# Performance work log

Measured on AMD Instinct MI355X. Metric: run time of the kernel, lower is better.

The kernel has to match this reference:

```python
import jax, jax.numpy as jnp
import numpy as np

N_HIDDEN = 512
N_MOTIF_PER_CLASS = 16
N_CLASS = 10
N_MOTIF = N_MOTIF_PER_CLASS * N_CLASS
TEMPERATURE = 0.2
EPS = 1e-4


def setup_inputs() -> dict:
    key = jax.random.key(0)
    k1, k2, k3 = jax.random.split(key, 3)
    B = 65536
    z = jax.random.normal(k1, (B, N_HIDDEN), dtype=jnp.float32)
    M = jax.random.normal(k2, (N_MOTIF, N_HIDDEN), dtype=jnp.float32)
    y = jax.random.randint(k3, (B,), 0, N_CLASS, dtype=jnp.int64)
    return {"z": z, "M": M, "y": y}


def reference(z, M, y):
    # euclidean_1 similarity: squared euclidean distance + log-ratio transform
    xp = z @ M.T                                     # [B, n_motif]
    dist = -2.0 * xp + jnp.sum(z * z, axis=1, keepdims=True) \
           + jnp.sum(M * M, axis=1)[None, :]         # [B, n_motif]
    similarity = jnp.log((dist + 1.0) / (dist + EPS))

    sims = jnp.exp(similarity / TEMPERATURE)          # [B, n_motif]

    # true_motifs mask: motif j belongs to class j // n_motif_per_class
    motif_class = jnp.arange(N_MOTIF) // N_MOTIF_PER_CLASS   # [n_motif]
    pos_mask = (motif_class[None, :] == y[:, None])           # [B, n_motif] bool

    # positives are contiguous per row, so the torch boolean-index reshape
    # is equivalent to a masked row-sum
    sim_pos = jnp.sum(jnp.where(pos_mask, sims, 0.0), axis=1)  # [B]
    sim_neg = jnp.sum(jnp.where(pos_mask, 0.0, sims), axis=1)  # [B]

    loss = -jnp.mean(jnp.log(sim_pos / (sim_neg + sim_pos)))
    return loss
```

## Files before the change

### kernel.cpp

```cpp
#include <hip/hip_runtime.h>
#include <math.h>

#define NH 512
#define NM 160
#define BROWS 65536
#define BM 128
#define BK 64
#define NCHUNK (NH / BK)

typedef __attribute__((ext_vector_type(8))) __bf16 bf16x8;
typedef __attribute__((ext_vector_type(4))) __bf16 bf16x4;
typedef __attribute__((ext_vector_type(4))) float  f32x4;

__global__ __launch_bounds__(64) void mprep_kernel(const float* __restrict__ M,
                                                   __bf16* __restrict__ Mb,
                                                   float* __restrict__ mnorm) {
    const int m = blockIdx.x;
    const int l = threadIdx.x;
    const float* row = M + (size_t)m * NH;
    float s = 0.f;
#pragma unroll
    for (int k = 0; k < 2; ++k) {
        float4 v = *reinterpret_cast<const float4*>(row + 4 * l + 256 * k);
        s = fmaf(v.x, v.x, fmaf(v.y, v.y, fmaf(v.z, v.z, fmaf(v.w, v.w, s))));
        bf16x4 b = {(__bf16)v.x, (__bf16)v.y, (__bf16)v.z, (__bf16)v.w};
        *reinterpret_cast<bf16x4*>(Mb + (size_t)m * NH + 4 * l + 256 * k) = b;
    }
#pragma unroll
    for (int off = 32; off > 0; off >>= 1) s += __shfl_down(s, off);
    if (l == 0) mnorm[m] = s;
}

__global__ __launch_bounds__(256, 2) void motif_main(
    const float* __restrict__ z, const __bf16* __restrict__ Mb,
    const int* __restrict__ y, const float* __restrict__ mnorm,
    float* __restrict__ loss_sum) {
    __shared__ __align__(16) __bf16 zs[BM * BK];
    __shared__ __align__(16) __bf16 ms[NM * BK];
    __shared__ float znorm[BM];
    __shared__ float red[256];

    const int tid = threadIdx.x;
    const int w   = tid >> 6;
    const int l   = tid & 63;
    const int row0 = blockIdx.x * BM;

    f32x4 acc[2][10];
#pragma unroll
    for (int rt = 0; rt < 2; ++rt)
#pragma unroll
        for (int ct = 0; ct < 10; ++ct) acc[rt][ct] = (f32x4){0.f, 0.f, 0.f, 0.f};
    float zp[8] = {0.f, 0.f, 0.f, 0.f, 0.f, 0.f, 0.f, 0.f};

#pragma unroll 1
    for (int ch = 0; ch < NCHUNK; ++ch) {
        const int k0 = ch * BK;
#pragma unroll
        for (int s = 0; s < 8; ++s) {
            const int idx = tid + 256 * s;
            const int r = idx >> 4, c4 = idx & 15;
            float4 v = *reinterpret_cast<const float4*>(
                z + (size_t)(row0 + r) * NH + k0 + c4 * 4);
            zp[s] = fmaf(v.x, v.x, fmaf(v.y, v.y, fmaf(v.z, v.z, fmaf(v.w, v.w, zp[s]))));
            const int slot = (c4 >> 1) ^ (r & 7);
            bf16x4 b = {(__bf16)v.x, (__bf16)v.y, (__bf16)v.z, (__bf16)v.w};
            *reinterpret_cast<bf16x4*>(&zs[r * BK + slot * 8 + (c4 & 1) * 4]) = b;
        }
#pragma unroll
        for (int s = 0; s < 5; ++s) {
            const int sidx = tid + 256 * s;
            const int r = sidx >> 3, sl = sidx & 7;
            bf16x8 v = *reinterpret_cast<const bf16x8*>(
                Mb + (size_t)r * NH + k0 + sl * 8);
            *reinterpret_cast<bf16x8*>(&ms[r * BK + (sl ^ (r & 7)) * 8]) = v;
        }
        __syncthreads();

        const int r16 = l & 15;
        const int kg  = l >> 4;
#pragma unroll
        for (int q = 0; q < 2; ++q) {
            const int slotk = q * 4 + kg;
            bf16x8 a[2], b[10];
#pragma unroll
            for (int rt = 0; rt < 2; ++rt) {
                const int r = w * 32 + rt * 16 + r16;
                a[rt] = *reinterpret_cast<const bf16x8*>(
                    &zs[r * BK + (slotk ^ (r & 7)) * 8]);
            }
#pragma unroll
            for (int ct = 0; ct < 10; ++ct) {
                const int r = ct * 16 + r16;
                b[ct] = *reinterpret_cast<const bf16x8*>(
                    &ms[r * BK + (slotk ^ (r & 7)) * 8]);
            }
#pragma unroll
            for (int rt = 0; rt < 2; ++rt)
#pragma unroll
                for (int ct = 0; ct < 10; ++ct)
                    acc[rt][ct] = __builtin_amdgcn_mfma_f32_16x16x32_bf16(
                        a[rt], b[ct], acc[rt][ct], 0, 0, 0);
        }
        __syncthreads();
    }

#pragma unroll
    for (int s = 0; s < 8; ++s) {
#pragma unroll
        for (int off = 1; off < 16; off <<= 1) zp[s] += __shfl_xor(zp[s], off);
    }
    if ((l & 15) == 0) {
#pragma unroll
        for (int s = 0; s < 8; ++s) znorm[(tid >> 4) + 16 * s] = zp[s];
    }
    __syncthreads();

    float mn[10];
#pragma unroll
    for (int ct = 0; ct < 10; ++ct) mn[ct] = mnorm[ct * 16 + (l & 15)];

    float local = 0.f;
#pragma unroll
    for (int rt = 0; rt < 2; ++rt) {
#pragma unroll
        for (int rr = 0; rr < 4; ++rr) {
            const int row = w * 32 + rt * 16 + (l >> 4) * 4 + rr;
            const float nz = znorm[row];
            const int yr = y[row0 + row];
            float p = 0.f, t = 0.f;
#pragma unroll
            for (int ct = 0; ct < 10; ++ct) {
                float dist = nz + mn[ct] - 2.0f * acc[rt][ct][rr];
                float rat = (dist + 1.0f) / (dist + 1e-4f);
                float r2 = rat * rat;
                float sv = r2 * r2 * rat;
                t += sv;
                p = (ct == yr) ? (p + sv) : p;
            }
#pragma unroll
            for (int off = 1; off < 16; off <<= 1) {
                p += __shfl_xor(p, off);
                t += __shfl_xor(t, off);
            }
            if ((l & 15) == 0) local += logf(p / t);
        }
    }

    red[tid] = local;
    __syncthreads();
#pragma unroll 1
    for (int s = 128; s > 0; s >>= 1) {
        if (tid < s) red[tid] += red[tid + s];
        __syncthreads();
    }
    if (tid == 0) atomicAdd(loss_sum, red[0]);
}

__global__ void finalize_kernel(const float* __restrict__ loss_sum,
                                float* __restrict__ out) {
    out[0] = -loss_sum[0] * (1.0f / (float)BROWS);
}

extern "C" void kernel_launch(void* const* d_in, const int* in_sizes, int n_in,
                              void* d_out, int out_size, void* d_ws, size_t ws_size,
                              hipStream_t stream) {
    const float* z = (const float*)d_in[0];
    const float* M = (const float*)d_in[1];
    const int*   y = (const int*)d_in[2];
    float* out = (float*)d_out;

    __bf16* Mb      = (__bf16*)d_ws;
    float*  mnorm   = (float*)((char*)d_ws + (size_t)NM * NH * sizeof(__bf16));
    float*  loss_sum = mnorm + NM;

    hipMemsetAsync(loss_sum, 0, sizeof(float), stream);
    mprep_kernel<<<NM, 64, 0, stream>>>(M, Mb, mnorm);
    motif_main<<<BROWS / BM, 256, 0, stream>>>(z, Mb, y, mnorm, loss_sum);
    finalize_kernel<<<1, 1, 0, stream>>>(loss_sum, out);
}
```

Measured before the change: 207.6 us.

## Register-prefetch next K chunk during MFMA and fold finalize into main kernel

Loads the next chunk of z and the bf16 motif matrix into registers right after the shared-memory stores, so global load latency overlaps with the MFMA work on the current chunk. It also removes the separate finalize launch: the last block to finish, detected with an atomic counter, writes the scaled loss. The cost is more live registers (8 float4 plus 5 bf16x8) under a 2-blocks-per-SM launch bound, which may cause spills or lower occupancy, and one extra atomic per block.

Result: no change. 209.4 us (+0.9%).

```diff
diff --git a/kernel.cpp b/kernel.cpp
--- a/kernel.cpp
+++ b/kernel.cpp
@@ -7,6 +7,7 @@
 #define BM 128
 #define BK 64
 #define NCHUNK (NH / BK)
+#define NBLK (BROWS / BM)
 
 typedef __attribute__((ext_vector_type(8))) __bf16 bf16x8;
 typedef __attribute__((ext_vector_type(4))) __bf16 bf16x4;
@@ -34,7 +35,8 @@
 __global__ __launch_bounds__(256, 2) void motif_main(
     const float* __restrict__ z, const __bf16* __restrict__ Mb,
     const int* __restrict__ y, const float* __restrict__ mnorm,
-    float* __restrict__ loss_sum) {
+    float* __restrict__ loss_sum, unsigned int* __restrict__ done_count,
+    float* __restrict__ out) {
     __shared__ __align__(16) __bf16 zs[BM * BK];
     __shared__ __align__(16) __bf16 ms[NM * BK];
     __shared__ float znorm[BM];
@@ -52,15 +54,29 @@
         for (int ct = 0; ct < 10; ++ct) acc[rt][ct] = (f32x4){0.f, 0.f, 0.f, 0.f};
     float zp[8] = {0.f, 0.f, 0.f, 0.f, 0.f, 0.f, 0.f, 0.f};
 
+    float4 pz[8];
+    bf16x8 pm[5];
+#pragma unroll
+    for (int s = 0; s < 8; ++s) {
+        const int idx = tid + 256 * s;
+        const int r = idx >> 4, c4 = idx & 15;
+        pz[s] = *reinterpret_cast<const float4*>(
+            z + (size_t)(row0 + r) * NH + c4 * 4);
+    }
+#pragma unroll
+    for (int s = 0; s < 5; ++s) {
+        const int sidx = tid + 256 * s;
+        const int r = sidx >> 3, sl = sidx & 7;
+        pm[s] = *reinterpret_cast<const bf16x8*>(Mb + (size_t)r * NH + sl * 8);
+    }
+
 #pragma unroll 1
     for (int ch = 0; ch < NCHUNK; ++ch) {
-        const int k0 = ch * BK;
 #pragma unroll
         for (int s = 0; s < 8; ++s) {
             const int idx = tid + 256 * s;
             const int r = idx >> 4, c4 = idx & 15;
-            float4 v = *reinterpret_cast<const float4*>(
-                z + (size_t)(row0 + r) * NH + k0 + c4 * 4);
+            const float4 v = pz[s];
             zp[s] = fmaf(v.x, v.x, fmaf(v.y, v.y, fmaf(v.z, v.z, fmaf(v.w, v.w, zp[s]))));
             const int slot = (c4 >> 1) ^ (r & 7);
             bf16x4 b = {(__bf16)v.x, (__bf16)v.y, (__bf16)v.z, (__bf16)v.w};
@@ -70,11 +86,27 @@
         for (int s = 0; s < 5; ++s) {
             const int sidx = tid + 256 * s;
             const int r = sidx >> 3, sl = sidx & 7;
-            bf16x8 v = *reinterpret_cast<const bf16x8*>(
-                Mb + (size_t)r * NH + k0 + sl * 8);
-            *reinterpret_cast<bf16x8*>(&ms[r * BK + (sl ^ (r & 7)) * 8]) = v;
+            *reinterpret_cast<bf16x8*>(&ms[r * BK + (sl ^ (r & 7)) * 8]) = pm[s];
         }
         __syncthreads();
+
+        if (ch + 1 < NCHUNK) {
+            const int k0n = (ch + 1) * BK;
+#pragma unroll
+            for (int s = 0; s < 8; ++s) {
+                const int idx = tid + 256 * s;
+                const int r = idx >> 4, c4 = idx & 15;
+                pz[s] = *reinterpret_cast<const float4*>(
+                    z + (size_t)(row0 + r) * NH + k0n + c4 * 4);
+            }
+#pragma unroll
+            for (int s = 0; s < 5; ++s) {
+                const int sidx = tid + 256 * s;
+                const int r = sidx >> 3, sl = sidx & 7;
+                pm[s] = *reinterpret_cast<const bf16x8*>(
+                    Mb + (size_t)r * NH + k0n + sl * 8);
+            }
+        }
 
         const int r16 = l & 15;
         const int kg  = l >> 4;
@@ -153,12 +185,16 @@
         if (tid < s) red[tid] += red[tid + s];
         __syncthreads();
     }
-    if (tid == 0) atomicAdd(loss_sum, red[0]);
-}
-
-__global__ void finalize_kernel(const float* __restrict__ loss_sum,
-                                float* __restrict__ out) {
-    out[0] = -loss_sum[0] * (1.0f / (float)BROWS);
+    if (tid == 0) {
+        atomicAdd(loss_sum, red[0]);
+        __threadfence();
+        unsigned prev = atomicAdd(done_count, 1u);
+        if (prev == (unsigned)(NBLK - 1)) {
+            __threadfence();
+            float total = atomicAdd(loss_sum, 0.0f);
+            out[0] = -total * (1.0f / (float)BROWS);
+        }
+    }
 }
 
 extern "C" void kernel_launch(void* const* d_in, const int* in_sizes, int n_in,
@@ -169,12 +205,12 @@
     const int*   y = (const int*)d_in[2];
     float* out = (float*)d_out;
 
-    __bf16* Mb      = (__bf16*)d_ws;
-    float*  mnorm   = (float*)((char*)d_ws + (size_t)NM * NH * sizeof(__bf16));
+    __bf16* Mb       = (__bf16*)d_ws;
+    float*  mnorm    = (float*)((char*)d_ws + (size_t)NM * NH * sizeof(__bf16));
     float*  loss_sum = mnorm + NM;
-
-    hipMemsetAsync(loss_sum, 0, sizeof(float), stream);
+    unsigned int* done_count = (unsigned int*)(loss_sum + 1);
+
+    hipMemsetAsync(loss_sum, 0, 2 * sizeof(float), stream);
     mprep_kernel<<<NM, 64, 0, stream>>>(M, Mb, mnorm);
-    motif_main<<<BROWS / BM, 256, 0, stream>>>(z, Mb, y, mnorm, loss_sum);
-    finalize_kernel<<<1, 1, 0, stream>>>(loss_sum, out);
+    motif_main<<<NBLK, 256, 0, stream>>>(z, Mb, y, mnorm, loss_sum, done_count, out);
 }
```

## Halve K-chunk, raise occupancy, fold finalize into main kernel via last-block reduction

Applied to the files above, without the earlier changes.

Shrinks the K chunk from 64 to 32, which halves shared memory per block and drops the XOR swizzle, and raises launch bounds to 3 blocks per CU. It also removes the separate finalize kernel by having the last block, detected with an atomic completion counter, write the final loss. The aim is more latency hiding on this memory-bound streaming of z and one fewer kernel launch. In exchange there are twice as many barriers per row tile, and LDS reads may now hit bank conflicts without the swizzle.

Result: slower. 218.8 us (+5.4%).

```diff
diff --git a/kernel.cpp b/kernel.cpp
--- a/kernel.cpp
+++ b/kernel.cpp
@@ -5,8 +5,9 @@
 #define NM 160
 #define BROWS 65536
 #define BM 128
-#define BK 64
+#define BK 32
 #define NCHUNK (NH / BK)
+#define NBLK (BROWS / BM)
 
 typedef __attribute__((ext_vector_type(8))) __bf16 bf16x8;
 typedef __attribute__((ext_vector_type(4))) __bf16 bf16x4;
@@ -31,10 +32,11 @@
     if (l == 0) mnorm[m] = s;
 }
 
-__global__ __launch_bounds__(256, 2) void motif_main(
+__global__ __launch_bounds__(256, 3) void motif_main(
     const float* __restrict__ z, const __bf16* __restrict__ Mb,
     const int* __restrict__ y, const float* __restrict__ mnorm,
-    float* __restrict__ loss_sum) {
+    float* __restrict__ loss_sum, unsigned int* __restrict__ done_count,
+    float* __restrict__ out) {
     __shared__ __align__(16) __bf16 zs[BM * BK];
     __shared__ __align__(16) __bf16 ms[NM * BK];
     __shared__ float znorm[BM];
@@ -50,68 +52,62 @@
     for (int rt = 0; rt < 2; ++rt)
 #pragma unroll
         for (int ct = 0; ct < 10; ++ct) acc[rt][ct] = (f32x4){0.f, 0.f, 0.f, 0.f};
-    float zp[8] = {0.f, 0.f, 0.f, 0.f, 0.f, 0.f, 0.f, 0.f};
+    float zp[4] = {0.f, 0.f, 0.f, 0.f};
 
 #pragma unroll 1
     for (int ch = 0; ch < NCHUNK; ++ch) {
         const int k0 = ch * BK;
 #pragma unroll
-        for (int s = 0; s < 8; ++s) {
+        for (int s = 0; s < 4; ++s) {
             const int idx = tid + 256 * s;
-            const int r = idx >> 4, c4 = idx & 15;
+            const int r = idx >> 3, c4 = idx & 7;
             float4 v = *reinterpret_cast<const float4*>(
                 z + (size_t)(row0 + r) * NH + k0 + c4 * 4);
             zp[s] = fmaf(v.x, v.x, fmaf(v.y, v.y, fmaf(v.z, v.z, fmaf(v.w, v.w, zp[s]))));
-            const int slot = (c4 >> 1) ^ (r & 7);
             bf16x4 b = {(__bf16)v.x, (__bf16)v.y, (__bf16)v.z, (__bf16)v.w};
-            *reinterpret_cast<bf16x4*>(&zs[r * BK + slot * 8 + (c4 & 1) * 4]) = b;
+            *reinterpret_cast<bf16x4*>(&zs[r * BK + c4 * 4]) = b;
         }
 #pragma unroll
-        for (int s = 0; s < 5; ++s) {
-            const int sidx = tid + 256 * s;
-            const int r = sidx >> 3, sl = sidx & 7;
-            bf16x8 v = *reinterpret_cast<const bf16x8*>(
-                Mb + (size_t)r * NH + k0 + sl * 8);
-            *reinterpret_cast<bf16x8*>(&ms[r * BK + (sl ^ (r & 7)) * 8]) = v;
+        for (int s = 0; s < 3; ++s) {
+            const int idx = tid + 256 * s;
+            if (idx < NM * 4) {
+                const int r = idx >> 2, sl = idx & 3;
+                bf16x8 v = *reinterpret_cast<const bf16x8*>(
+                    Mb + (size_t)r * NH + k0 + sl * 8);
+                *reinterpret_cast<bf16x8*>(&ms[r * BK + sl * 8]) = v;
+            }
         }
         __syncthreads();
 
         const int r16 = l & 15;
         const int kg  = l >> 4;
+        bf16x8 a[2];
 #pragma unroll
-        for (int q = 0; q < 2; ++q) {
-            const int slotk = q * 4 + kg;
-            bf16x8 a[2], b[10];
+        for (int rt = 0; rt < 2; ++rt)
+            a[rt] = *reinterpret_cast<const bf16x8*>(
+                &zs[(w * 32 + rt * 16 + r16) * BK + kg * 8]);
 #pragma unroll
-            for (int rt = 0; rt < 2; ++rt) {
-                const int r = w * 32 + rt * 16 + r16;
-                a[rt] = *reinterpret_cast<const bf16x8*>(
-                    &zs[r * BK + (slotk ^ (r & 7)) * 8]);
-            }
+        for (int h = 0; h < 2; ++h) {
+            bf16x8 b[5];
 #pragma unroll
-            for (int ct = 0; ct < 10; ++ct) {
-                const int r = ct * 16 + r16;
-                b[ct] = *reinterpret_cast<const bf16x8*>(
-                    &ms[r * BK + (slotk ^ (r & 7)) * 8]);
-            }
+            for (int j = 0; j < 5; ++j)
+                b[j] = *reinterpret_cast<const bf16x8*>(
+                    &ms[((h * 5 + j) * 16 + r16) * BK + kg * 8]);
 #pragma unroll
             for (int rt = 0; rt < 2; ++rt)
 #pragma unroll
-                for (int ct = 0; ct < 10; ++ct)
-                    acc[rt][ct] = __builtin_amdgcn_mfma_f32_16x16x32_bf16(
-                        a[rt], b[ct], acc[rt][ct], 0, 0, 0);
+                for (int j = 0; j < 5; ++j)
+                    acc[rt][h * 5 + j] = __builtin_amdgcn_mfma_f32_16x16x32_bf16(
+                        a[rt], b[j], acc[rt][h * 5 + j], 0, 0, 0);
         }
         __syncthreads();
     }
 
 #pragma unroll
-    for (int s = 0; s < 8; ++s) {
+    for (int s = 0; s < 4; ++s) {
 #pragma unroll
-        for (int off = 1; off < 16; off <<= 1) zp[s] += __shfl_xor(zp[s], off);
-    }
-    if ((l & 15) == 0) {
-#pragma unroll
-        for (int s = 0; s < 8; ++s) znorm[(tid >> 4) + 16 * s] = zp[s];
+        for (int off = 1; off < 8; off <<= 1) zp[s] += __shfl_xor(zp[s], off);
+        if ((l & 7) == 0) znorm[(tid + 256 * s) >> 3] = zp[s];
     }
     __syncthreads();
 
@@ -153,12 +149,16 @@
         if (tid < s) red[tid] += red[tid + s];
         __syncthreads();
     }
-    if (tid == 0) atomicAdd(loss_sum, red[0]);
-}
-
-__global__ void finalize_kernel(const float* __restrict__ loss_sum,
-                                float* __restrict__ out) {
-    out[0] = -loss_sum[0] * (1.0f / (float)BROWS);
+    if (tid == 0) {
+        atomicAdd(loss_sum, red[0]);
+        __threadfence();
+        unsigned prev = atomicAdd(done_count, 1u);
+        if (prev == (unsigned)(NBLK - 1)) {
+            __threadfence();
+            float total = atomicAdd(loss_sum, 0.0f);
+            out[0] = -total * (1.0f / (float)BROWS);
+        }
+    }
 }
 
 extern "C" void kernel_launch(void* const* d_in, const int* in_sizes, int n_in,
@@ -169,12 +169,12 @@
     const int*   y = (const int*)d_in[2];
     float* out = (float*)d_out;
 
-    __bf16* Mb      = (__bf16*)d_ws;
-    float*  mnorm   = (float*)((char*)d_ws + (size_t)NM * NH * sizeof(__bf16));
+    __bf16* Mb       = (__bf16*)d_ws;
+    float*  mnorm    = (float*)((char*)d_ws + (size_t)NM * NH * sizeof(__bf16));
     float*  loss_sum = mnorm + NM;
+    unsigned int* done_count = (unsigned int*)(loss_sum + 1);
 
-    hipMemsetAsync(loss_sum, 0, sizeof(float), stream);
+    hipMemsetAsync(loss_sum, 0, 2 * sizeof(float), stream);
     mprep_kernel<<<NM, 64, 0, stream>>>(M, Mb, mnorm);
-    motif_main<<<BROWS / BM, 256, 0, stream>>>(z, Mb, y, mnorm, loss_sum);
-    finalize_kernel<<<1, 1, 0, stream>>>(loss_sum, out);
+    motif_main<<<NBLK, 256, 0, stream>>>(z, Mb, y, mnorm, loss_sum, done_count, out);
 }
```

## Halve block tile to 64 rows with 128 threads and fuse finalize via last-block

Applied to the files above, without the earlier changes.

Shrinks each block to 64 rows and 2 waves, doubling the grid to 1024 blocks and raising the occupancy hint to 3 blocks per CU, so there are more blocks to spread across CUs. The separate finalize kernel is removed: a done counter lets the last block to finish write the mean loss, saving one launch. In exchange, every block now loads the full 160-row motif tile per chunk for half as many rows, which doubles the redundant M traffic and LDS fill work per row. Fence ordering around the atomics adds a little tail latency.

After: 258.9 us. +24.7%, slower.

```diff
diff --git a/kernel.cpp b/kernel.cpp
--- a/kernel.cpp
+++ b/kernel.cpp
@@ -4,9 +4,11 @@
 #define NH 512
 #define NM 160
 #define BROWS 65536
-#define BM 128
+#define BM 64
 #define BK 64
+#define NT 128
 #define NCHUNK (NH / BK)
+#define NBLK (BROWS / BM)
 
 typedef __attribute__((ext_vector_type(8))) __bf16 bf16x8;
 typedef __attribute__((ext_vector_type(4))) __bf16 bf16x4;
@@ -31,14 +33,15 @@
     if (l == 0) mnorm[m] = s;
 }
 
-__global__ __launch_bounds__(256, 2) void motif_main(
+__global__ __launch_bounds__(NT, 3) void motif_main(
     const float* __restrict__ z, const __bf16* __restrict__ Mb,
     const int* __restrict__ y, const float* __restrict__ mnorm,
-    float* __restrict__ loss_sum) {
+    float* __restrict__ loss_sum, unsigned int* __restrict__ done_count,
+    float* __restrict__ out) {
     __shared__ __align__(16) __bf16 zs[BM * BK];
     __shared__ __align__(16) __bf16 ms[NM * BK];
     __shared__ float znorm[BM];
-    __shared__ float red[256];
+    __shared__ float red[NT];
 
     const int tid = threadIdx.x;
     const int w   = tid >> 6;
@@ -57,7 +60,7 @@
         const int k0 = ch * BK;
 #pragma unroll
         for (int s = 0; s < 8; ++s) {
-            const int idx = tid + 256 * s;
+            const int idx = tid + NT * s;
             const int r = idx >> 4, c4 = idx & 15;
             float4 v = *reinterpret_cast<const float4*>(
                 z + (size_t)(row0 + r) * NH + k0 + c4 * 4);
@@ -67,8 +70,8 @@
             *reinterpret_cast<bf16x4*>(&zs[r * BK + slot * 8 + (c4 & 1) * 4]) = b;
         }
 #pragma unroll
-        for (int s = 0; s < 5; ++s) {
-            const int sidx = tid + 256 * s;
+        for (int s = 0; s < 10; ++s) {
+            const int sidx = tid + NT * s;
             const int r = sidx >> 3, sl = sidx & 7;
             bf16x8 v = *reinterpret_cast<const bf16x8*>(
                 Mb + (size_t)r * NH + k0 + sl * 8);
@@ -108,10 +111,7 @@
     for (int s = 0; s < 8; ++s) {
 #pragma unroll
         for (int off = 1; off < 16; off <<= 1) zp[s] += __shfl_xor(zp[s], off);
-    }
-    if ((l & 15) == 0) {
-#pragma unroll
-        for (int s = 0; s < 8; ++s) znorm[(tid >> 4) + 16 * s] = zp[s];
+        if ((l & 15) == 0) znorm[s * 8 + (tid >> 4)] = zp[s];
     }
     __syncthreads();
 
@@ -149,16 +149,20 @@
     red[tid] = local;
     __syncthreads();
 #pragma unroll 1
-    for (int s = 128; s > 0; s >>= 1) {
+    for (int s = NT / 2; s > 0; s >>= 1) {
         if (tid < s) red[tid] += red[tid + s];
         __syncthreads();
     }
-    if (tid == 0) atomicAdd(loss_sum, red[0]);
-}
-
-__global__ void finalize_kernel(const float* __restrict__ loss_sum,
-                                float* __restrict__ out) {
-    out[0] = -loss_sum[0] * (1.0f / (float)BROWS);
+    if (tid == 0) {
+        atomicAdd(loss_sum, red[0]);
+        __threadfence();
+        unsigned prev = atomicAdd(done_count, 1u);
+        if (prev == (unsigned)(NBLK - 1)) {
+            __threadfence();
+            float total = atomicAdd(loss_sum, 0.0f);
+            out[0] = -total * (1.0f / (float)BROWS);
+        }
+    }
 }
 
 extern "C" void kernel_launch(void* const* d_in, const int* in_sizes, int n_in,
@@ -169,12 +173,12 @@
     const int*   y = (const int*)d_in[2];
     float* out = (float*)d_out;
 
-    __bf16* Mb      = (__bf16*)d_ws;
-    float*  mnorm   = (float*)((char*)d_ws + (size_t)NM * NH * sizeof(__bf16));
+    __bf16* Mb       = (__bf16*)d_ws;
+    float*  mnorm    = (float*)((char*)d_ws + (size_t)NM * NH * sizeof(__bf16));
     float*  loss_sum = mnorm + NM;
+    unsigned int* done_count = (unsigned int*)(loss_sum + 1);
 
-    hipMemsetAsync(loss_sum, 0, sizeof(float), stream);
+    hipMemsetAsync(loss_sum, 0, 2 * sizeof(float), stream);
     mprep_kernel<<<NM, 64, 0, stream>>>(M, Mb, mnorm);
-    motif_main<<<BROWS / BM, 256, 0, stream>>>(z, Mb, y, mnorm, loss_sum);
-    finalize_kernel<<<1, 1, 0, stream>>>(loss_sum, out);
+    motif_main<<<NBLK, NT, 0, stream>>>(z, Mb, y, mnorm, loss_sum, done_count, out);
 }
```
